# Kernel tuning notes

Hardware: AMD Instinct MI355X
Metric: run time of the kernel (lower is better)

The kernel has to match this reference:

```python
import jax, jax.numpy as jnp
import numpy as np

NB_BINS = 10
N = 33554432  # number of predictions


def setup_inputs() -> dict:
    key = jax.random.key(0)
    k1, k2 = jax.random.split(key)
    logits = jax.random.normal(k1, (N,), dtype=jnp.float32)
    labels = jax.random.randint(k2, (N,), 0, 2, dtype=jnp.int32)
    return {"logits": logits, "labels": labels}


def reference(logits, labels):
    nb = NB_BINS
    conf = jax.nn.sigmoid(logits)
    # Bin b covers (b/nb, (b+1)/nb]: conf > lower & conf <= upper.
    # ceil(conf*nb)-1 maps exact boundary k/nb to bin k-1, matching gt/le.
    # sigmoid output is strictly in (0,1) for finite logits, so clip is safe.
    bins = jnp.clip(jnp.ceil(conf * nb).astype(jnp.int32) - 1, 0, nb - 1)

    counts = jax.ops.segment_sum(jnp.ones_like(conf), bins, num_segments=nb)
    label_sum = jax.ops.segment_sum(labels.astype(conf.dtype), bins, num_segments=nb)
    conf_sum = jax.ops.segment_sum(conf, bins, num_segments=nb)

    nonempty = counts > 0
    denom = jnp.where(nonempty, counts, 1.0)
    positives_per_bin = jnp.where(nonempty, label_sum / denom, 0.0)
    confidence_per_bin = jnp.where(nonempty, conf_sum / denom, 0.0)

    ece_i = jnp.where(nonempty, jnp.abs(positives_per_bin - confidence_per_bin), 0.0)
    ece = jnp.sum(ece_i)
    max_ece = jnp.max(ece_i)  # original inits max_ece=0, zeros for empty bins match
    return positives_per_bin, confidence_per_bin, ece, max_ece
```

## Files before the change

kernel.cpp:

```cpp
#include <hip/hip_runtime.h>

#define NB 10
#define BLOCK 256
#define GRID 4096
#define K 8


typedef float vfloat4 __attribute__((ext_vector_type(4)));
typedef int   vint4   __attribute__((ext_vector_type(4)));

__device__ __forceinline__ void acc_one(float xx, unsigned ll,
                                        unsigned long long& cnt64,
                                        unsigned long long& lab64,
                                        unsigned long long& rA,
                                        unsigned long long& rB) {
    float e = __expf(-xx);
    float conf = __builtin_amdgcn_rcpf(1.0f + e);
    float t = conf * 10.0f;
    int b = (int)t;
    b = min(b, NB - 1);
    float r = t - (float)b;
    unsigned rfix = (unsigned)__builtin_fmaf(r, 63.0f, 0.5f);
    int s6 = b * 6;
    cnt64 += 1ULL << s6;
    lab64 += (unsigned long long)ll << s6;
    bool hi = b >= 5;
    int s12 = (hi ? b - 5 : b) * 12;
    unsigned long long val = (unsigned long long)rfix << s12;
    rA += hi ? 0ULL : val;
    rB += hi ? val : 0ULL;
}

__device__ __forceinline__ void flush_packed(unsigned long long& cnt64,
                                             unsigned long long& lab64,
                                             unsigned long long& rA,
                                             unsigned long long& rB,
                                             unsigned* cl, unsigned* ru) {
#pragma unroll
    for (int i = 0; i < NB; ++i) {
        unsigned c = (unsigned)((cnt64 >> (6 * i)) & 63ULL);
        unsigned l = (unsigned)((lab64 >> (6 * i)) & 63ULL);
        cl[i] += c | (l << 16);
    }
#pragma unroll
    for (int i = 0; i < 5; ++i) {
        ru[i]     += (unsigned)((rA >> (12 * i)) & 4095ULL);
        ru[5 + i] += (unsigned)((rB >> (12 * i)) & 4095ULL);
    }
    cnt64 = 0ULL; lab64 = 0ULL; rA = 0ULL; rB = 0ULL;
}

__global__ __launch_bounds__(BLOCK) void ece_partial(const float* __restrict__ logits,
                                                     const int* __restrict__ labels,
                                                     unsigned int* __restrict__ ws,
                                                     int n, int wstride) {
    const int tid = threadIdx.x;
    const int n4 = n >> 2;
    const vfloat4* __restrict__ l4 = (const vfloat4*)logits;
    const vint4*   __restrict__ b4 = (const vint4*)labels;

    unsigned cl[NB], ru[NB];
#pragma unroll
    for (int i = 0; i < NB; ++i) { cl[i] = 0u; ru[i] = 0u; }

    const int TILE = BLOCK * K;
    for (int tbase = blockIdx.x * TILE; tbase < n4; tbase += GRID * TILE) {
        unsigned long long cnt64 = 0ULL, lab64 = 0ULL, rA = 0ULL, rB = 0ULL;
        if (tbase + TILE <= n4) {
            vfloat4 x[K];
            vint4   y[K];
            const int base = tbase + tid;
#pragma unroll
            for (int k = 0; k < K; ++k) x[k] = __builtin_nontemporal_load(&l4[base + k * BLOCK]);
#pragma unroll
            for (int k = 0; k < K; ++k) y[k] = __builtin_nontemporal_load(&b4[base + k * BLOCK]);
#pragma unroll
            for (int k = 0; k < K; ++k) {
#pragma unroll
                for (int j = 0; j < 4; ++j)
                    acc_one(x[k][j], (unsigned)y[k][j], cnt64, lab64, rA, rB);
            }
        } else {
            for (int k = 0; k < K; ++k) {
                int idx = tbase + tid + k * BLOCK;
                if (idx < n4) {
                    vfloat4 x = __builtin_nontemporal_load(&l4[idx]);
                    vint4   yv = __builtin_nontemporal_load(&b4[idx]);
#pragma unroll
                    for (int j = 0; j < 4; ++j)
                        acc_one(x[j], (unsigned)yv[j], cnt64, lab64, rA, rB);
                }
            }
        }
        flush_packed(cnt64, lab64, rA, rB, cl, ru);
    }
    if (blockIdx.x == 0 && tid == 0 && (n & 3)) {
        unsigned long long cnt64 = 0ULL, lab64 = 0ULL, rA = 0ULL, rB = 0ULL;
        for (int j2 = n4 * 4; j2 < n; ++j2)
            acc_one(logits[j2], (unsigned)labels[j2], cnt64, lab64, rA, rB);
        flush_packed(cnt64, lab64, rA, rB, cl, ru);
    }

#pragma unroll
    for (int i = 0; i < NB; ++i) {
#pragma unroll
        for (int off = 32; off > 0; off >>= 1) {
            cl[i] += __shfl_down(cl[i], off, 64);
            ru[i] += __shfl_down(ru[i], off, 64);
        }
    }

    __shared__ unsigned red[4][2 * NB];
    const int wave = tid >> 6, lane = tid & 63;
    if (lane == 0) {
#pragma unroll
        for (int i = 0; i < NB; ++i) { red[wave][i] = cl[i]; red[wave][NB + i] = ru[i]; }
    }
    __syncthreads();
    if (tid < 2 * NB) {
        unsigned s = red[0][tid] + red[1][tid] + red[2][tid] + red[3][tid];
        if (tid < NB) {
            atomicAdd(&ws[tid * wstride], s & 0xffffu);
            atomicAdd(&ws[(NB + tid) * wstride], s >> 16);
        } else {
            atomicAdd(&ws[(NB + tid) * wstride], s);
        }
    }
}

__global__ void ece_final(const unsigned int* __restrict__ ws, float* __restrict__ out,
                          int wstride) {
    if (threadIdx.x == 0 && blockIdx.x == 0) {
        float ece = 0.0f, mx = 0.0f;
        for (int b = 0; b < NB; ++b) {
            unsigned cnt = ws[b * wstride];
            unsigned lab = ws[(NB + b) * wstride];
            unsigned rs  = ws[(2 * NB + b) * wstride];
            float pos = 0.0f, cfb = 0.0f, e = 0.0f;
            if (cnt > 0u) {
                float inv = 1.0f / (float)cnt;
                pos = (float)lab * inv;
                cfb = ((float)b + (float)rs * (1.0f / 63.0f) * inv) * 0.1f;
                e = fabsf(pos - cfb);
            }
            out[b] = pos;
            out[NB + b] = cfb;
            ece += e;
            mx = fmaxf(mx, e);
        }
        out[2 * NB] = ece;
        out[2 * NB + 1] = mx;
    }
}

extern "C" void kernel_launch(void* const* d_in, const int* in_sizes, int n_in,
                              void* d_out, int out_size, void* d_ws, size_t ws_size,
                              hipStream_t stream) {
    const float* logits = (const float*)d_in[0];
    const int*   labels = (const int*)d_in[1];
    float* out = (float*)d_out;
    unsigned int* ws = (unsigned int*)d_ws;
    int n = in_sizes[0];

    int wstride = (ws_size >= 30 * 16 * sizeof(unsigned)) ? 16 : 1;
    hipMemsetAsync(d_ws, 0, (size_t)(30 * wstride) * sizeof(unsigned), stream);

    ece_partial<<<GRID, BLOCK, 0, stream>>>(logits, labels, ws, n, wstride);
    ece_final<<<1, 64, 0, stream>>>(ws, out, wstride);
}
```

Before: 302.5 us.

## Issue all loads up front with grid-stride layout and fused sigmoid scaling

Reworks the main kernel so each thread handles exactly 16 float4 vectors (grid of 2048 blocks) when n matches the expected size. It issues all 32 vector loads before any compute, with a scheduling barrier to keep them together, and keeps a generic grid-stride fallback for other sizes. It also folds the sigmoid and the ×10 scaling into a single fma plus reciprocal. The aim is more memory-level parallelism and fewer instructions, at the cost of high register pressure under launch_bounds(256,2).

```diff
diff --git a/kernel.cpp b/kernel.cpp
--- a/kernel.cpp
+++ b/kernel.cpp
@@ -2,8 +2,8 @@
 
 #define NB 10
 #define BLOCK 256
-#define GRID 4096
-#define K 8
+#define GRID 2048
+#define SSTRIDE (GRID * BLOCK)
 
 
 typedef float vfloat4 __attribute__((ext_vector_type(4)));
@@ -15,8 +15,7 @@
                                         unsigned long long& rA,
                                         unsigned long long& rB) {
     float e = __expf(-xx);
-    float conf = __builtin_amdgcn_rcpf(1.0f + e);
-    float t = conf * 10.0f;
+    float t = __builtin_amdgcn_rcpf(__builtin_fmaf(e, 0.1f, 0.1f));
     int b = (int)t;
     b = min(b, NB - 1);
     float r = t - (float)b;
@@ -50,11 +49,12 @@
     cnt64 = 0ULL; lab64 = 0ULL; rA = 0ULL; rB = 0ULL;
 }
 
-__global__ __launch_bounds__(BLOCK) void ece_partial(const float* __restrict__ logits,
-                                                     const int* __restrict__ labels,
-                                                     unsigned int* __restrict__ ws,
-                                                     int n, int wstride) {
+__global__ __launch_bounds__(BLOCK, 2) void ece_partial(const float* __restrict__ logits,
+                                                        const int* __restrict__ labels,
+                                                        unsigned int* __restrict__ ws,
+                                                        int n, int wstride) {
     const int tid = threadIdx.x;
+    const int gtid = blockIdx.x * BLOCK + tid;
     const int n4 = n >> 2;
     const vfloat4* __restrict__ l4 = (const vfloat4*)logits;
     const vint4*   __restrict__ b4 = (const vint4*)labels;
@@ -63,42 +63,50 @@
 #pragma unroll
     for (int i = 0; i < NB; ++i) { cl[i] = 0u; ru[i] = 0u; }
 
-    const int TILE = BLOCK * K;
-    for (int tbase = blockIdx.x * TILE; tbase < n4; tbase += GRID * TILE) {
+    if (n4 == 16 * SSTRIDE) {
+        vfloat4 x0[8], x1[8];
+        vint4   y0[8], y1[8];
+#pragma unroll
+        for (int j = 0; j < 8; ++j) x0[j] = __builtin_nontemporal_load(&l4[gtid + j * SSTRIDE]);
+#pragma unroll
+        for (int j = 0; j < 8; ++j) y0[j] = __builtin_nontemporal_load(&b4[gtid + j * SSTRIDE]);
+#pragma unroll
+        for (int j = 0; j < 8; ++j) x1[j] = __builtin_nontemporal_load(&l4[gtid + (8 + j) * SSTRIDE]);
+#pragma unroll
+        for (int j = 0; j < 8; ++j) y1[j] = __builtin_nontemporal_load(&b4[gtid + (8 + j) * SSTRIDE]);
+        __builtin_amdgcn_sched_barrier(0);
+
         unsigned long long cnt64 = 0ULL, lab64 = 0ULL, rA = 0ULL, rB = 0ULL;
-        if (tbase + TILE <= n4) {
-            vfloat4 x[K];
-            vint4   y[K];
-            const int base = tbase + tid;
 #pragma unroll
-            for (int k = 0; k < K; ++k) x[k] = __builtin_nontemporal_load(&l4[base + k * BLOCK]);
+        for (int j = 0; j < 8; ++j) {
 #pragma unroll
-            for (int k = 0; k < K; ++k) y[k] = __builtin_nontemporal_load(&b4[base + k * BLOCK]);
-#pragma unroll
-            for (int k = 0; k < K; ++k) {
-#pragma unroll
-                for (int j = 0; j < 4; ++j)
-                    acc_one(x[k][j], (unsigned)y[k][j], cnt64, lab64, rA, rB);
-            }
-        } else {
-            for (int k = 0; k < K; ++k) {
-                int idx = tbase + tid + k * BLOCK;
-                if (idx < n4) {
-                    vfloat4 x = __builtin_nontemporal_load(&l4[idx]);
-                    vint4   yv = __builtin_nontemporal_load(&b4[idx]);
-#pragma unroll
-                    for (int j = 0; j < 4; ++j)
-                        acc_one(x[j], (unsigned)yv[j], cnt64, lab64, rA, rB);
-                }
-            }
+            for (int k = 0; k < 4; ++k)
+                acc_one(x0[j][k], (unsigned)y0[j][k], cnt64, lab64, rA, rB);
         }
         flush_packed(cnt64, lab64, rA, rB, cl, ru);
-    }
-    if (blockIdx.x == 0 && tid == 0 && (n & 3)) {
-        unsigned long long cnt64 = 0ULL, lab64 = 0ULL, rA = 0ULL, rB = 0ULL;
-        for (int j2 = n4 * 4; j2 < n; ++j2)
-            acc_one(logits[j2], (unsigned)labels[j2], cnt64, lab64, rA, rB);
+#pragma unroll
+        for (int j = 0; j < 8; ++j) {
+#pragma unroll
+            for (int k = 0; k < 4; ++k)
+                acc_one(x1[j][k], (unsigned)y1[j][k], cnt64, lab64, rA, rB);
+        }
         flush_packed(cnt64, lab64, rA, rB, cl, ru);
+    } else {
+        for (int v = gtid; v < n4; v += SSTRIDE) {
+            unsigned long long cnt64 = 0ULL, lab64 = 0ULL, rA = 0ULL, rB = 0ULL;
+            vfloat4 x = __builtin_nontemporal_load(&l4[v]);
+            vint4   y = __builtin_nontemporal_load(&b4[v]);
+#pragma unroll
+            for (int k = 0; k < 4; ++k)
+                acc_one(x[k], (unsigned)y[k], cnt64, lab64, rA, rB);
+            flush_packed(cnt64, lab64, rA, rB, cl, ru);
+        }
+        if (gtid == 0 && (n & 3)) {
+            unsigned long long cnt64 = 0ULL, lab64 = 0ULL, rA = 0ULL, rB = 0ULL;
+            for (int j2 = n4 * 4; j2 < n; ++j2)
+                acc_one(logits[j2], (unsigned)labels[j2], cnt64, lab64, rA, rB);
+            flush_packed(cnt64, lab64, rA, rB, cl, ru);
+        }
     }
 
 #pragma unroll
```

New measurement: 275.6 us. 1.1x faster.
